# Performance work log

Hardware: AMD Instinct MI355X
Metric: run time of the kernel (lower is better)

The kernel has to match this reference:

```python
import jax, jax.numpy as jnp
import numpy as np

N = 100000
E = 1000000
IN_DIM = 256
HID = 128
LAYERS = 8
ALPHA = 0.1
THETA = 0.5


def setup_inputs() -> dict:
    key = jax.random.key(0)
    ks = jax.random.split(key, 12)
    x = jax.random.normal(ks[0], (N, IN_DIM), dtype=jnp.float32)
    edge_index = jax.random.randint(ks[1], (2, E), 0, N, dtype=jnp.int64)
    s1 = 1.0 / np.sqrt(IN_DIM)
    s2 = 1.0 / np.sqrt(HID)
    W1 = jax.random.normal(ks[2], (IN_DIM, HID), dtype=jnp.float32) * s1
    b1 = jnp.zeros((HID,), dtype=jnp.float32)
    conv_w = jax.random.normal(ks[3], (LAYERS, HID, HID), dtype=jnp.float32) * s2
    W2 = jax.random.normal(ks[4], (HID, HID), dtype=jnp.float32) * s2
    b2 = jnp.zeros((HID,), dtype=jnp.float32)
    Wv = jax.random.normal(ks[5], (HID, HID), dtype=jnp.float32) * s2
    bv = jnp.zeros((HID,), dtype=jnp.float32)
    Wt = jax.random.normal(ks[6], (HID, HID), dtype=jnp.float32) * s2
    bt = jnp.zeros((HID,), dtype=jnp.float32)
    return {"x": x, "edge_index": edge_index, "W1": W1, "b1": b1,
            "conv_w": conv_w, "W2": W2, "b2": b2, "Wv": Wv, "bv": bv,
            "Wt": Wt, "bt": bt}


def _gcn_norm(edge_index, n):
    # add self-loops, symmetric normalization (PyG gcn_norm defaults)
    loop = jnp.arange(n, dtype=edge_index.dtype)
    src = jnp.concatenate([edge_index[0], loop])
    dst = jnp.concatenate([edge_index[1], loop])
    deg = jax.ops.segment_sum(jnp.ones_like(dst, dtype=jnp.float32), dst, num_segments=n)
    dinv = jnp.where(deg > 0, jax.lax.rsqrt(jnp.maximum(deg, 1.0)), 0.0)
    norm = dinv[src] * dinv[dst]  # [E+N]
    return src, dst, norm


def reference(x, edge_index, W1, b1, conv_w, W2, b2, Wv, bv, Wt, bt):
    n = x.shape[0]
    src, dst, norm = _gcn_norm(edge_index, n)
    h = jax.nn.relu(x @ W1 + b1)          # [N, HID]
    h0 = h
    for l in range(conv_w.shape[0]):
        beta = float(np.log(THETA / (l + 1) + 1.0))
        # sparse neighborhood aggregation: gather -> scale -> scatter-add
        agg = jax.ops.segment_sum(h[src] * norm[:, None], dst, num_segments=n)
        comb = (1.0 - ALPHA) * agg + ALPHA * h0   # initial residual
        h = jax.nn.relu((1.0 - beta) * comb + beta * (comb @ conv_w[l]))
    out = h @ W2 + b2
    x_vision = jax.nn.relu(out @ Wv + bv)
    x_text = jax.nn.relu(out @ Wt + bt)
    return (out, x_vision, x_text)
```

## Files before the change

kernel.cpp:

```cpp
#include <hip/hip_runtime.h>
#include <hip/hip_fp16.h>
#include <math.h>

#define NN 100000
#define NE 1000000
#define IND 256
#define HD  128
#define HD2 64
#define NPB 32
#define FNPB 64
#define INPB 64
#define NBLK_SCAN 98
#define ECAP 768
#define H16_BYTES ((size_t)NN * HD * 2)

typedef _Float16 f16x8 __attribute__((ext_vector_type(8)));
typedef float f32x4 __attribute__((ext_vector_type(4)));

union U16 { uint4 u; __half2 h2[4]; __half h[8]; f16x8 v; };


__global__ __launch_bounds__(256) void k_deg(const int* __restrict__ dst,
                                             int* __restrict__ deg) {
    int e = blockIdx.x * 256 + threadIdx.x;
    if (e < NE) atomicAdd(&deg[dst[e]], 1);
}

__global__ __launch_bounds__(256) void k_dinv(const int* __restrict__ deg,
                                              float* __restrict__ dinv) {
    int i = blockIdx.x * 256 + threadIdx.x;
    if (i < NN) dinv[i] = rsqrtf((float)(deg[i] + 1));
}

__global__ __launch_bounds__(1024) void k_scan1(const int* __restrict__ deg,
                                                int* __restrict__ rowp,
                                                int* __restrict__ bsums) {
    __shared__ int s[1024];
    int t = threadIdx.x;
    int i = blockIdx.x * 1024 + t;
    int v = (i < NN) ? deg[i] : 0;
    s[t] = v;
    __syncthreads();
    for (int off = 1; off < 1024; off <<= 1) {
        int u = (t >= off) ? s[t - off] : 0;
        __syncthreads();
        s[t] += u;
        __syncthreads();
    }
    if (i < NN) rowp[i] = s[t] - v;
    if (t == 1023) bsums[blockIdx.x] = s[1023];
}

__global__ __launch_bounds__(128) void k_scan2(int* __restrict__ bsums) {
    __shared__ int s[128];
    int t = threadIdx.x;
    int v = (t < NBLK_SCAN) ? bsums[t] : 0;
    s[t] = v;
    __syncthreads();
    for (int off = 1; off < 128; off <<= 1) {
        int u = (t >= off) ? s[t - off] : 0;
        __syncthreads();
        s[t] += u;
        __syncthreads();
    }
    if (t < NBLK_SCAN) bsums[t] = s[t] - v;
}

__global__ __launch_bounds__(1024) void k_scan3(int* __restrict__ rowp,
                                                const int* __restrict__ bsums) {
    int i = blockIdx.x * 1024 + threadIdx.x;
    if (i < NN) rowp[i] += bsums[i >> 10];
    if (i == 0) rowp[NN] = NE;
}

__global__ __launch_bounds__(256) void k_fill(const int* __restrict__ src,
                                              const int* __restrict__ dst,
                                              const int* __restrict__ rowp,
                                              int* __restrict__ fill,
                                              int* __restrict__ col) {
    int e = blockIdx.x * 256 + threadIdx.x;
    if (e < NE) {
        int d = dst[e];
        int pos = rowp[d] + atomicAdd(&fill[d], 1);
        col[pos] = src[e];
    }
}


__global__ __launch_bounds__(256) void k_wfrag(const float* __restrict__ cw,
                                               const float* __restrict__ W2,
                                               const float* __restrict__ Wv,
                                               const float* __restrict__ Wt,
                                               __half* __restrict__ wf) {
    int m = blockIdx.x >> 4;
    int blk = blockIdx.x & 15;
    const float* W = (m < 8) ? (cw + (size_t)m * HD * HD)
                             : (m == 8 ? W2 : (m == 9 ? Wv : Wt));
    int i = (blk * 256 + threadIdx.x) * 4;
    float4 v = *(const float4*)&W[i];
    int k = i >> 7, col0 = i & 127;
    float vv[4] = {v.x, v.y, v.z, v.w};
    __half* dstm = wf + (size_t)m * HD * HD;
    int ks = k >> 5, laneK = ((k >> 3) & 3) * 16, j = k & 7;
#pragma unroll
    for (int t = 0; t < 4; t++) {
        int col = col0 + t;
        int nt = col >> 4;
        int lane = laneK + (col & 15);
        dstm[((nt * 4 + ks) * 64 + lane) * 8 + j] = __float2half(vv[t]);
    }
}


__global__ __launch_bounds__(256) void k_w1frag(const float* __restrict__ W1,
                                                __half* __restrict__ w1f) {
    int i = (blockIdx.x * 256 + threadIdx.x) * 4;
    float4 v = *(const float4*)&W1[i];
    int k = i >> 7, col0 = i & 127;
    float vv[4] = {v.x, v.y, v.z, v.w};
    int ks = k >> 5, laneK = ((k >> 3) & 3) * 16, j = k & 7;
#pragma unroll
    for (int t = 0; t < 4; t++) {
        int col = col0 + t;
        int nt = col >> 4;
        int lane = laneK + (col & 15);
        w1f[((nt * 8 + ks) * 64 + lane) * 8 + j] = __float2half(vv[t]);
    }
}


__global__ __launch_bounds__(256) void k_init(const float* __restrict__ x,
                                              const __half* __restrict__ w1f,
                                              const float* __restrict__ b1,
                                              const float* __restrict__ dinv,
                                              __half* __restrict__ h0h,
                                              __half* __restrict__ g0) {
    __shared__ char lds[32768];
    int tid = threadIdx.x;
    int nb = blockIdx.x * INPB;
    int wv = tid >> 6, lane = tid & 63;

#pragma unroll
    for (int it = 0; it < 8; it++) {
        int c = it * 256 + tid;
        int row = c >> 5, k8 = c & 31;
        int gn = nb + row;
        float4 a = make_float4(0.f, 0.f, 0.f, 0.f), b = a;
        if (gn < NN) {
            a = *(const float4*)&x[(size_t)gn * IND + k8 * 8];
            b = *(const float4*)&x[(size_t)gn * IND + k8 * 8 + 4];
        }
        U16 p;
        p.h[0] = __float2half(a.x); p.h[1] = __float2half(a.y);
        p.h[2] = __float2half(a.z); p.h[3] = __float2half(a.w);
        p.h[4] = __float2half(b.x); p.h[5] = __float2half(b.y);
        p.h[6] = __float2half(b.z); p.h[7] = __float2half(b.w);
        int byte = (row * 512 + k8 * 16) ^ ((row & 7) << 4);
        *(uint4*)(lds + byte) = p.u;
    }
    __syncthreads();

    int arow = wv * 16 + (lane & 15);
    f16x8 a[8];
#pragma unroll
    for (int ks = 0; ks < 8; ks++) {
        int byte = (arow * 512 + ks * 64 + (lane >> 4) * 16) ^ ((arow & 7) << 4);
        U16 r; r.u = *(const uint4*)(lds + byte);
        a[ks] = r.v;
    }
    __syncthreads();

    __half* hb = (__half*)lds;
    __half* gbuf = (__half*)(lds + 16384);
    const uint4* bf = (const uint4*)w1f;

#pragma unroll
    for (int nt = 0; nt < 8; nt++) {
        f32x4 acc = {0.f, 0.f, 0.f, 0.f};
#pragma unroll
        for (int ks = 0; ks < 8; ks++) {
            U16 bw; bw.u = bf[(nt * 8 + ks) * 64 + lane];
            acc = __builtin_amdgcn_mfma_f32_16x16x32_f16(a[ks], bw.v, acc, 0, 0, 0);
        }
        int colb = nt * 16 + (lane & 15);
        float bias = b1[colb];
#pragma unroll
        for (int r = 0; r < 4; r++) {
            int row = wv * 16 + (lane >> 4) * 4 + r;
            int gn = nb + row;
            float dv = (gn < NN) ? dinv[gn] : 0.f;
            float v = fmaxf(acc[r] + bias, 0.f);
            hb[row * HD + colb] = __float2half(v);
            gbuf[row * HD + colb] = __float2half(dv * v);
        }
    }
    __syncthreads();

#pragma unroll
    for (int it = 0; it < 4; it++) {
        int c = it * 256 + tid;
        int row = c >> 4;
        if (nb + row < NN) {
            *(uint4*)((char*)h0h + (size_t)nb * 256 + c * 16) = *(uint4*)((char*)hb + c * 16);
            *(uint4*)((char*)g0 + (size_t)nb * 256 + c * 16) = *(uint4*)((char*)gbuf + c * 16);
        }
    }
}


template <int OUT_MODE>
__global__ __launch_bounds__(256) void k_layer(const __half2* __restrict__ gIn,
                                               __half* __restrict__ gOutH,
                                               float* __restrict__ hOut,
                                               const __half2* __restrict__ h0,
                                               const float* __restrict__ dinv,
                                               const int* __restrict__ rowp,
                                               const int* __restrict__ col,
                                               const __half* __restrict__ wfL,
                                               float beta) {
    __shared__ float cs[NPB * HD];
    __shared__ __half csh[NPB * HD];
    __shared__ int sCol[ECAP];
    __shared__ int sRowp[NPB + 1];
    __shared__ int sCtr;
    int tid = threadIdx.x;
    int nb = blockIdx.x * NPB;
    int lane = tid & 63;
    int sub = lane & 15;
    const uint4* g4 = (const uint4*)gIn;
    const uint4* h4 = (const uint4*)h0;

    if (tid == 0) sCtr = 0;
    if (tid <= NPB) sRowp[tid] = rowp[nb + tid];
    __syncthreads();
    int base = sRowp[0];
    int total = sRowp[NPB] - base;
    int stct = total < ECAP ? total : ECAP;
    for (int i = tid; i < stct; i += 256) sCol[i] = col[base + i];
    __syncthreads();

    while (true) {
        int nl;
        if (sub == 0) nl = atomicAdd(&sCtr, 1);
        nl = __shfl(nl, lane & 48);
        if (nl >= NPB) break;
        int n = nb + nl;
        int beg = sRowp[nl] - base, end = sRowp[nl + 1] - base;

        float acc[8];
        {
            U16 v; v.u = g4[(size_t)n * 16 + sub];
#pragma unroll
            for (int q = 0; q < 4; q++) {
                float2 f = __half22float2(v.h2[q]);
                acc[2 * q] = f.x; acc[2 * q + 1] = f.y;
            }
        }

        int e = beg;
        for (; e + 4 <= end; e += 4) {
            int c0 = (e     < ECAP) ? sCol[e]     : col[base + e];
            int c1 = (e + 1 < ECAP) ? sCol[e + 1] : col[base + e + 1];
            int c2 = (e + 2 < ECAP) ? sCol[e + 2] : col[base + e + 2];
            int c3 = (e + 3 < ECAP) ? sCol[e + 3] : col[base + e + 3];
            U16 a0, a1, a2, a3;
            a0.u = g4[(size_t)c0 * 16 + sub];
            a1.u = g4[(size_t)c1 * 16 + sub];
            a2.u = g4[(size_t)c2 * 16 + sub];
            a3.u = g4[(size_t)c3 * 16 + sub];
#pragma unroll
            for (int q = 0; q < 4; q++) {
                float2 f0 = __half22float2(a0.h2[q]);
                float2 f1 = __half22float2(a1.h2[q]);
                float2 f2 = __half22float2(a2.h2[q]);
                float2 f3 = __half22float2(a3.h2[q]);
                acc[2 * q]     += (f0.x + f1.x) + (f2.x + f3.x);
                acc[2 * q + 1] += (f0.y + f1.y) + (f2.y + f3.y);
            }
        }
        if (e + 2 <= end) {
            int c0 = (e     < ECAP) ? sCol[e]     : col[base + e];
            int c1 = (e + 1 < ECAP) ? sCol[e + 1] : col[base + e + 1];
            U16 a0, a1;
            a0.u = g4[(size_t)c0 * 16 + sub];
            a1.u = g4[(size_t)c1 * 16 + sub];
#pragma unroll
            for (int q = 0; q < 4; q++) {
                float2 f0 = __half22float2(a0.h2[q]);
                float2 f1 = __half22float2(a1.h2[q]);
                acc[2 * q]     += f0.x + f1.x;
                acc[2 * q + 1] += f0.y + f1.y;
            }
            e += 2;
        }
        if (e < end) {
            int c0 = (e < ECAP) ? sCol[e] : col[base + e];
            U16 a0; a0.u = g4[(size_t)c0 * 16 + sub];
#pragma unroll
            for (int q = 0; q < 4; q++) {
                float2 f0 = __half22float2(a0.h2[q]);
                acc[2 * q] += f0.x; acc[2 * q + 1] += f0.y;
            }
        }

        float dv = dinv[n];
        U16 hv; hv.u = h4[(size_t)n * 16 + sub];
        float co[8];
        U16 p;
#pragma unroll
        for (int q = 0; q < 4; q++) {
            float2 hf = __half22float2(hv.h2[q]);
            co[2 * q]     = 0.9f * dv * acc[2 * q]     + 0.1f * hf.x;
            co[2 * q + 1] = 0.9f * dv * acc[2 * q + 1] + 0.1f * hf.y;
            p.h2[q] = __float22half2_rn(make_float2(co[2 * q], co[2 * q + 1]));
        }
        *(float4*)&cs[nl * HD + sub * 8]     = make_float4(co[0], co[1], co[2], co[3]);
        *(float4*)&cs[nl * HD + sub * 8 + 4] = make_float4(co[4], co[5], co[6], co[7]);
        int fbyte = (nl * 256 + sub * 16) ^ ((nl & 7) << 4);
        *(uint4*)((char*)csh + fbyte) = p.u;
    }
    __syncthreads();

    int wave = tid >> 6;
    int rt = wave >> 1;
    int ntb = (wave & 1) * 4;
    int arow = rt * 16 + (lane & 15);
    f16x8 a[4];
#pragma unroll
    for (int ks = 0; ks < 4; ks++) {
        int byte = (arow * 256 + ks * 64 + (lane >> 4) * 16) ^ ((arow & 7) << 4);
        U16 r; r.u = *(const uint4*)((const char*)csh + byte);
        a[ks] = r.v;
    }
    __syncthreads();

    const uint4* bf = (const uint4*)wfL;
    float omb = 1.f - beta;
#pragma unroll
    for (int nt2 = 0; nt2 < 4; nt2++) {
        int nt = ntb + nt2;
        f32x4 acc = {0.f, 0.f, 0.f, 0.f};
#pragma unroll
        for (int ks = 0; ks < 4; ks++) {
            U16 bw; bw.u = bf[(nt * 4 + ks) * 64 + lane];
            acc = __builtin_amdgcn_mfma_f32_16x16x32_f16(a[ks], bw.v, acc, 0, 0, 0);
        }
        int colb = nt * 16 + (lane & 15);
#pragma unroll
        for (int r = 0; r < 4; r++) {
            int row = rt * 16 + (lane >> 4) * 4 + r;
            int gn = nb + row;
            float comb = cs[row * HD + colb];
            float v = fmaxf(omb * comb + beta * acc[r], 0.f);
            if (OUT_MODE == 0) {
                csh[row * HD + colb] = __float2half(dinv[gn] * v);
            } else {
                hOut[(size_t)gn * HD + colb] = v;
            }
        }
    }
    if (OUT_MODE == 0) {
        __syncthreads();
#pragma unroll
        for (int it = 0; it < 2; it++) {
            int c = it * 256 + tid;
            *(uint4*)((char*)gOutH + (size_t)nb * 256 + c * 16) =
                *(uint4*)((char*)csh + c * 16);
        }
    }
}


__global__ __launch_bounds__(256) void k_final(const float* __restrict__ hIn,
                                               const __half* __restrict__ wf,
                                               const float* __restrict__ b2,
                                               const float* __restrict__ bv,
                                               const float* __restrict__ bt,
                                               float* __restrict__ out,
                                               float* __restrict__ vis,
                                               float* __restrict__ txt) {
    __shared__ __half hs[FNPB * HD];
    __shared__ __half os[FNPB * HD];
    int tid = threadIdx.x;
    int nb = blockIdx.x * FNPB;
    int wave = tid >> 6, lane = tid & 63;

#pragma unroll
    for (int it = 0; it < 4; it++) {
        int idx8 = it * 256 + tid;
        int row = idx8 >> 4, c8 = idx8 & 15;
        int gn = nb + row;
        float4 a = make_float4(0.f, 0.f, 0.f, 0.f), b = a;
        if (gn < NN) {
            a = *(const float4*)&hIn[(size_t)gn * HD + c8 * 8];
            b = *(const float4*)&hIn[(size_t)gn * HD + c8 * 8 + 4];
        }
        U16 p;
        p.h[0] = __float2half(a.x); p.h[1] = __float2half(a.y);
        p.h[2] = __float2half(a.z); p.h[3] = __float2half(a.w);
        p.h[4] = __float2half(b.x); p.h[5] = __float2half(b.y);
        p.h[6] = __float2half(b.z); p.h[7] = __float2half(b.w);
        int byte = (row * 256 + c8 * 16) ^ ((row & 7) << 4);
        *(uint4*)((char*)hs + byte) = p.u;
    }
    __syncthreads();

    const uint4* bf2 = (const uint4*)(wf + (size_t)8 * HD * HD);
    const uint4* bfv = (const uint4*)(wf + (size_t)9 * HD * HD);
    const uint4* bft = (const uint4*)(wf + (size_t)10 * HD * HD);

    int arow = wave * 16 + (lane & 15);
    int kb = (lane >> 4) * 8;

    f16x8 a[4];
#pragma unroll
    for (int ks = 0; ks < 4; ks++) {
        int byte = (arow * 256 + (ks * 32 + kb) * 2) ^ ((arow & 7) << 4);
        U16 r; r.u = *(const uint4*)((const char*)hs + byte);
        a[ks] = r.v;
    }

#pragma unroll
    for (int nt = 0; nt < 8; nt++) {
        f32x4 acc = {0.f, 0.f, 0.f, 0.f};
#pragma unroll
        for (int ks = 0; ks < 4; ks++) {
            U16 bw; bw.u = bf2[(nt * 4 + ks) * 64 + lane];
            acc = __builtin_amdgcn_mfma_f32_16x16x32_f16(a[ks], bw.v, acc, 0, 0, 0);
        }
        int c = nt * 16 + (lane & 15);
        float bias = b2[c];
#pragma unroll
        for (int r = 0; r < 4; r++) {
            int lrow = wave * 16 + (lane >> 4) * 4 + r;
            float val = acc[r] + bias;
            int gn = nb + lrow;
            if (gn < NN) out[(size_t)gn * HD + c] = val;
            int byte = (lrow * 256 + c * 2) ^ ((lrow & 7) << 4);
            *(__half*)((char*)os + byte) = __float2half(val);
        }
    }
    __syncthreads();

    f16x8 ao[4];
#pragma unroll
    for (int ks = 0; ks < 4; ks++) {
        int byte = (arow * 256 + (ks * 32 + kb) * 2) ^ ((arow & 7) << 4);
        U16 r; r.u = *(const uint4*)((const char*)os + byte);
        ao[ks] = r.v;
    }

#pragma unroll
    for (int nt = 0; nt < 8; nt++) {
        f32x4 accv = {0.f, 0.f, 0.f, 0.f};
        f32x4 acct = {0.f, 0.f, 0.f, 0.f};
#pragma unroll
        for (int ks = 0; ks < 4; ks++) {
            U16 bwv; bwv.u = bfv[(nt * 4 + ks) * 64 + lane];
            U16 bwt; bwt.u = bft[(nt * 4 + ks) * 64 + lane];
            accv = __builtin_amdgcn_mfma_f32_16x16x32_f16(ao[ks], bwv.v, accv, 0, 0, 0);
            acct = __builtin_amdgcn_mfma_f32_16x16x32_f16(ao[ks], bwt.v, acct, 0, 0, 0);
        }
        int c = nt * 16 + (lane & 15);
        float biasv = bv[c], biast = bt[c];
#pragma unroll
        for (int r = 0; r < 4; r++) {
            int lrow = wave * 16 + (lane >> 4) * 4 + r;
            int gn = nb + lrow;
            if (gn < NN) {
                vis[(size_t)gn * HD + c] = fmaxf(accv[r] + biasv, 0.f);
                txt[(size_t)gn * HD + c] = fmaxf(acct[r] + biast, 0.f);
            }
        }
    }
}


extern "C" void kernel_launch(void* const* d_in, const int* in_sizes, int n_in,
                              void* d_out, int out_size, void* d_ws, size_t ws_size,
                              hipStream_t stream) {
    (void)in_sizes; (void)n_in; (void)out_size; (void)ws_size;

    const float* x    = (const float*)d_in[0];
    const int*   edge = (const int*)d_in[1];
    const float* W1   = (const float*)d_in[2];
    const float* b1   = (const float*)d_in[3];
    const float* cw   = (const float*)d_in[4];
    const float* W2   = (const float*)d_in[5];
    const float* b2   = (const float*)d_in[6];
    const float* Wv   = (const float*)d_in[7];
    const float* bv   = (const float*)d_in[8];
    const float* Wt   = (const float*)d_in[9];
    const float* bt   = (const float*)d_in[10];

    const int* esrc = edge;
    const int* edst = edge + NE;

    float* out0 = (float*)d_out;
    float* reg1 = out0 + (size_t)NN * HD;
    float* reg2 = reg1 + (size_t)NN * HD;

    __half* h0h = (__half*)reg1;
    __half* ga  = (__half*)reg2;
    __half* gb  = (__half*)((char*)reg2 + H16_BYTES);

    char* ws = (char*)d_ws;
    int*   deg_i = (int*)(ws + 0);
    int*   fill  = (int*)(ws + 400000);
    int*   rowp  = (int*)(ws + 800000);
    int*   bsums = (int*)(ws + 1200128);
    int*   col   = (int*)(ws + 1200640);
    float* dinv  = (float*)(ws + 5200640);
    __half* wf   = (__half*)(ws + 5600640);
    __half* w1f  = (__half*)(ws + 5961088);

    hipMemsetAsync(ws, 0, 800000, stream);

    k_deg<<<(NE + 255) / 256, 256, 0, stream>>>(edst, deg_i);
    k_dinv<<<(NN + 255) / 256, 256, 0, stream>>>(deg_i, dinv);
    k_scan1<<<NBLK_SCAN, 1024, 0, stream>>>(deg_i, rowp, bsums);
    k_scan2<<<1, 128, 0, stream>>>(bsums);
    k_scan3<<<NBLK_SCAN, 1024, 0, stream>>>(rowp, bsums);
    k_fill<<<(NE + 255) / 256, 256, 0, stream>>>(esrc, edst, rowp, fill, col);
    k_wfrag<<<11 * 16, 256, 0, stream>>>(cw, W2, Wv, Wt, wf);
    k_w1frag<<<32, 256, 0, stream>>>(W1, w1f);

    k_init<<<(NN + INPB - 1) / INPB, 256, 0, stream>>>(x, w1f, b1, dinv, h0h, ga);

    for (int l = 0; l < 7; l++) {
        float beta = (float)log(0.5 / (double)(l + 1) + 1.0);
        const __half* gi = (l & 1) ? gb : ga;
        __half*       go = (l & 1) ? ga : gb;
        k_layer<0><<<NN / NPB, 256, 0, stream>>>((const __half2*)gi, go,
                                                 (float*)nullptr, (const __half2*)h0h,
                                                 dinv, rowp, col,
                                                 wf + (size_t)l * HD * HD, beta);
    }
    {
        float beta = (float)log(0.5 / 8.0 + 1.0);
        k_layer<1><<<NN / NPB, 256, 0, stream>>>((const __half2*)gb, (__half*)nullptr,
                                                 out0, (const __half2*)h0h,
                                                 dinv, rowp, col,
                                                 wf + (size_t)7 * HD * HD, beta);
    }

    k_final<<<(NN + FNPB - 1) / FNPB, 256, 0, stream>>>(out0, wf, b2, bv, bt,
                                                        out0, reg1, reg2);
}
```

Before: 639.6 us.

## Fold residual blend into conv weights and store last layer as fp16

```diff
diff --git a/kernel.cpp b/kernel.cpp
--- a/kernel.cpp
+++ b/kernel.cpp
@@ -100,14 +100,20 @@
     float4 v = *(const float4*)&W[i];
     int k = i >> 7, col0 = i & 127;
     float vv[4] = {v.x, v.y, v.z, v.w};
+    float beta = 1.f, omb = 0.f;
+    if (m < 8) {
+        beta = logf(0.5f / (float)(m + 1) + 1.0f);
+        omb = 1.f - beta;
+    }
     __half* dstm = wf + (size_t)m * HD * HD;
     int ks = k >> 5, laneK = ((k >> 3) & 3) * 16, j = k & 7;
 #pragma unroll
     for (int t = 0; t < 4; t++) {
         int col = col0 + t;
+        float val = beta * vv[t] + ((k == col) ? omb : 0.f);
         int nt = col >> 4;
         int lane = laneK + (col & 15);
-        dstm[((nt * 4 + ks) * 64 + lane) * 8 + j] = __float2half(vv[t]);
+        dstm[((nt * 4 + ks) * 64 + lane) * 8 + j] = __float2half(val);
     }
 }
 
@@ -211,14 +217,12 @@
 template <int OUT_MODE>
 __global__ __launch_bounds__(256) void k_layer(const __half2* __restrict__ gIn,
                                                __half* __restrict__ gOutH,
-                                               float* __restrict__ hOut,
+                                               __half* __restrict__ hOut7,
                                                const __half2* __restrict__ h0,
                                                const float* __restrict__ dinv,
                                                const int* __restrict__ rowp,
                                                const int* __restrict__ col,
-                                               const __half* __restrict__ wfL,
-                                               float beta) {
-    __shared__ float cs[NPB * HD];
+                                               const __half* __restrict__ wfL) {
     __shared__ __half csh[NPB * HD];
     __shared__ int sCol[ECAP];
     __shared__ int sRowp[NPB + 1];
@@ -305,17 +309,14 @@
 
         float dv = dinv[n];
         U16 hv; hv.u = h4[(size_t)n * 16 + sub];
-        float co[8];
         U16 p;
 #pragma unroll
         for (int q = 0; q < 4; q++) {
             float2 hf = __half22float2(hv.h2[q]);
-            co[2 * q]     = 0.9f * dv * acc[2 * q]     + 0.1f * hf.x;
-            co[2 * q + 1] = 0.9f * dv * acc[2 * q + 1] + 0.1f * hf.y;
-            p.h2[q] = __float22half2_rn(make_float2(co[2 * q], co[2 * q + 1]));
-        }
-        *(float4*)&cs[nl * HD + sub * 8]     = make_float4(co[0], co[1], co[2], co[3]);
-        *(float4*)&cs[nl * HD + sub * 8 + 4] = make_float4(co[4], co[5], co[6], co[7]);
+            float c0 = 0.9f * dv * acc[2 * q]     + 0.1f * hf.x;
+            float c1 = 0.9f * dv * acc[2 * q + 1] + 0.1f * hf.y;
+            p.h2[q] = __float22half2_rn(make_float2(c0, c1));
+        }
         int fbyte = (nl * 256 + sub * 16) ^ ((nl & 7) << 4);
         *(uint4*)((char*)csh + fbyte) = p.u;
     }
@@ -335,7 +336,6 @@
     __syncthreads();
 
     const uint4* bf = (const uint4*)wfL;
-    float omb = 1.f - beta;
 #pragma unroll
     for (int nt2 = 0; nt2 < 4; nt2++) {
         int nt = ntb + nt2;
@@ -350,28 +350,35 @@
         for (int r = 0; r < 4; r++) {
             int row = rt * 16 + (lane >> 4) * 4 + r;
             int gn = nb + row;
-            float comb = cs[row * HD + colb];
-            float v = fmaxf(omb * comb + beta * acc[r], 0.f);
+            float v = fmaxf(acc[r], 0.f);
             if (OUT_MODE == 0) {
                 csh[row * HD + colb] = __float2half(dinv[gn] * v);
             } else {
-                hOut[(size_t)gn * HD + colb] = v;
+                csh[row * HD + colb] = __float2half(v);
             }
         }
     }
+    __syncthreads();
     if (OUT_MODE == 0) {
-        __syncthreads();
 #pragma unroll
         for (int it = 0; it < 2; it++) {
             int c = it * 256 + tid;
             *(uint4*)((char*)gOutH + (size_t)nb * 256 + c * 16) =
                 *(uint4*)((char*)csh + c * 16);
         }
-    }
-}
-
-
-__global__ __launch_bounds__(256) void k_final(const float* __restrict__ hIn,
+    } else {
+#pragma unroll
+        for (int it = 0; it < 2; it++) {
+            int c = it * 256 + tid;
+            int row = c >> 4;
+            *(uint4*)((char*)hOut7 + ((size_t)(nb + row) * 512 + (c & 15) * 16)) =
+                *(uint4*)((char*)csh + c * 16);
+        }
+    }
+}
+
+
+__global__ __launch_bounds__(256) void k_final(const __half* __restrict__ hIn,
                                                const __half* __restrict__ wf,
                                                const float* __restrict__ b2,
                                                const float* __restrict__ bv,
@@ -387,21 +394,14 @@
 
 #pragma unroll
     for (int it = 0; it < 4; it++) {
-        int idx8 = it * 256 + tid;
-        int row = idx8 >> 4, c8 = idx8 & 15;
+        int idx = it * 256 + tid;
+        int row = idx >> 4, c8 = idx & 15;
         int gn = nb + row;
-        float4 a = make_float4(0.f, 0.f, 0.f, 0.f), b = a;
-        if (gn < NN) {
-            a = *(const float4*)&hIn[(size_t)gn * HD + c8 * 8];
-            b = *(const float4*)&hIn[(size_t)gn * HD + c8 * 8 + 4];
-        }
-        U16 p;
-        p.h[0] = __float2half(a.x); p.h[1] = __float2half(a.y);
-        p.h[2] = __float2half(a.z); p.h[3] = __float2half(a.w);
-        p.h[4] = __float2half(b.x); p.h[5] = __float2half(b.y);
-        p.h[6] = __float2half(b.z); p.h[7] = __float2half(b.w);
+        uint4 p = make_uint4(0, 0, 0, 0);
+        if (gn < NN)
+            p = *(const uint4*)((const char*)hIn + (size_t)gn * 512 + c8 * 16);
         int byte = (row * 256 + c8 * 16) ^ ((row & 7) << 4);
-        *(uint4*)((char*)hs + byte) = p.u;
+        *(uint4*)((char*)hs + byte) = p;
     }
     __syncthreads();
 
@@ -528,22 +528,19 @@
     k_init<<<(NN + INPB - 1) / INPB, 256, 0, stream>>>(x, w1f, b1, dinv, h0h, ga);
 
     for (int l = 0; l < 7; l++) {
-        float beta = (float)log(0.5 / (double)(l + 1) + 1.0);
         const __half* gi = (l & 1) ? gb : ga;
         __half*       go = (l & 1) ? ga : gb;
         k_layer<0><<<NN / NPB, 256, 0, stream>>>((const __half2*)gi, go,
-                                                 (float*)nullptr, (const __half2*)h0h,
+                                                 (__half*)nullptr, (const __half2*)h0h,
                                                  dinv, rowp, col,
-                                                 wf + (size_t)l * HD * HD, beta);
-    }
-    {
-        float beta = (float)log(0.5 / 8.0 + 1.0);
-        k_layer<1><<<NN / NPB, 256, 0, stream>>>((const __half2*)gb, (__half*)nullptr,
-                                                 out0, (const __half2*)h0h,
-                                                 dinv, rowp, col,
-                                                 wf + (size_t)7 * HD * HD, beta);
-    }
-
-    k_final<<<(NN + FNPB - 1) / FNPB, 256, 0, stream>>>(out0, wf, b2, bv, bt,
+                                                 wf + (size_t)l * HD * HD);
+    }
+    k_layer<1><<<NN / NPB, 256, 0, stream>>>((const __half2*)gb, (__half*)nullptr,
+                                             (__half*)out0, (const __half2*)h0h,
+                                             dinv, rowp, col,
+                                             wf + (size_t)7 * HD * HD);
+
+    k_final<<<(NN + FNPB - 1) / FNPB, 256, 0, stream>>>((const __half*)out0, wf,
+                                                        b2, bv, bt,
                                                         out0, reg1, reg2);
 }
```

Result: faster. 612.1 us (-4.3%).
